# Kernel optimization log

Measured on AMD Instinct MI355X. Metric: run time of the kernel, lower is better.

The kernel has to match this reference:

```python
import jax, jax.numpy as jnp
import numpy as np

NEG_INF = -1e30  # stand-in for -inf pooling pad (matches torch max_pool2d implicit -inf pad)


def _max_pool(x, wh, ww, ph, pw):
    # x: (N, C, H, W); 'same'-style explicit padding as in torch max_pool2d
    return jax.lax.reduce_window(
        x, -jnp.inf, jax.lax.max,
        window_dimensions=(1, 1, wh, ww),
        window_strides=(1, 1, 1, 1),
        padding=((0, 0), (0, 0), (ph, ph), (pw, pw)))


def soft_erode(img):
    p1 = -_max_pool(-img, 3, 1, 1, 0)
    p2 = -_max_pool(-img, 1, 3, 0, 1)
    return jnp.minimum(p1, p2)


def soft_dilate(img):
    return _max_pool(img, 3, 3, 1, 1)


def soft_open(img):
    return soft_dilate(soft_erode(img))


def soft_skel(img, n_iter=50):
    skel = jax.nn.relu(img - soft_open(img))

    def body(carry, _):
        img, skel = carry
        img = soft_erode(img)
        delta = jax.nn.relu(img - soft_open(img))
        skel = skel + jax.nn.relu(delta - skel * delta)
        return (img, skel), None

    (_, skel), _ = jax.lax.scan(body, (img, skel), None, length=n_iter)
    return skel


def setup_inputs() -> dict:
    key = jax.random.key(0)
    k1, k2 = jax.random.split(key)
    N, C, H, W = 8, 1, 512, 512
    output = jax.random.normal(k1, (N, C, H, W), dtype=jnp.float32)
    target = jax.random.uniform(k2, (N, C, H, W), dtype=jnp.float32)
    return {"output": output, "target": target}


def reference(output, target):
    smooth = 1.0
    alpha = 0.7
    n_iter = 50
    axes = (1, 2, 3)  # per-sample reduction over C, H, W

    p = jax.nn.sigmoid(output)

    # soft clDice (vectorized over batch; original loops per sample with identical math)
    s_p = soft_skel(p, n_iter)
    s_l = soft_skel(target, n_iter)
    tprec = (jnp.sum(s_p * target, axes) + smooth) / (jnp.sum(s_p, axes) + smooth)
    tsens = (jnp.sum(s_l * p, axes) + smooth) / (jnp.sum(s_l, axes) + smooth)
    cl_dice = jnp.mean(1.0 - 2.0 * tprec * tsens / (tprec + tsens))

    # soft Dice
    inter = jnp.sum(p * target, axes)
    dice = jnp.mean(1.0 - 2.0 * (inter + smooth) /
                    (jnp.sum(p, axes) + jnp.sum(target, axes) + smooth))

    return alpha * dice + (1.0 - alpha) * cl_dice
```

## Files before the change

kernel.cpp:

```cpp
#include <hip/hip_runtime.h>
#include <math.h>

#define IMG   512
#define NSAMP 8
#define NIMG  16
#define PS    (IMG * IMG)

#define NBANDS 16
#define BH     (IMG / NBANDS)

__device__ __forceinline__ float sigm(float x) { return 1.0f / (1.0f + expf(-x)); }

__device__ __forceinline__ float dpp_a(float x) {
#if __has_builtin(__builtin_amdgcn_update_dpp)
    return __int_as_float(__builtin_amdgcn_update_dpp(0, __float_as_int(x),
                                                      0x130, 0xF, 0xF, true));
#else
    return __shfl_down(x, 1, 64);
#endif
}
__device__ __forceinline__ float dpp_b(float x) {
#if __has_builtin(__builtin_amdgcn_update_dpp)
    return __int_as_float(__builtin_amdgcn_update_dpp(0, __float_as_int(x),
                                                      0x138, 0xF, 0xF, true));
#else
    return __shfl_up(x, 1, 64);
#endif
}

__global__ __launch_bounds__(256) void prep_kernel(const float4* __restrict__ lg,
                                                   const float4* __restrict__ tg,
                                                   float4* __restrict__ X, int n4)
{
    int i = blockIdx.x * 256 + threadIdx.x;
    if (i < n4) {
        float4 L = lg[i];
        X[i]      = make_float4(sigm(L.x), sigm(L.y), sigm(L.z), sigm(L.w));
        X[i + n4] = tg[i];
    }
}

template<int C, bool ER, bool EC, bool INIT>
__device__ __forceinline__ void pipe_run(const float* __restrict__ xg,
                                         float* __restrict__ xo,
                                         float* __restrict__ Sg,
                                         int R0, int R1, int gcol, bool colOK, bool owned)
{
    const float INF = __builtin_inff();
    float A[C], B[C], HMA[C], HMB[C], SK[C];
    #pragma unroll
    for (int l = 0; l < C; ++l) {
        A[l] = INF; B[l] = INF; HMA[l] = -INF; HMB[l] = -INF; SK[l] = 0.f;
    }
    const int t0 = R0 - C - 1, t1 = R1 + C;

    auto xload = [&](int r) -> float {
        if (ER || EC) {
            bool ok = true;
            if (ER) ok = ok && ((unsigned)r < (unsigned)IMG);
            if (EC) ok = ok && colOK;
            float v = INF;
            if (ok) v = xg[r * IMG + gcol];
            return v;
        }
        return xg[r * IMG + gcol];
    };
    auto sload = [&](int r) -> float {
        if (INIT) return 0.f;
        if (ER || EC) {
            bool ok = true;
            if (ER) ok = ok && ((unsigned)r < (unsigned)IMG);
            if (EC) ok = ok && colOK;
            float v = 0.f;
            if (ok) v = Sg[r * IMG + gcol];
            return v;
        }
        return Sg[r * IMG + gcol];
    };

    float X0a = xload(t0), X0b = xload(t0 + 1);
    float SNa = sload(t0 - 1), SNb = sload(t0);

    #pragma unroll 2
    for (int t = t0; t <= t1; ++t) {
        float Cin = X0a; X0a = X0b; X0b = xload(t + 2);

        #pragma unroll
        for (int l = 0; l < C; ++l) {
            float Acur = A[l], Bcur = B[l];
            float e = fminf(fminf(Acur, Cin), Bcur);
            e = fminf(e, dpp_a(Bcur));
            e = fminf(e, dpp_b(Bcur));
            if (ER) e = ((unsigned)(t - l - 1) < (unsigned)IMG) ? e : INF;
            float eraw = e, xd = eraw;
            if (EC) {
                e  = colOK ? eraw :  INF;
                xd = colOK ? eraw : -INF;
            }
            float hm = fmaxf(xd, dpp_a(xd));
            hm = fmaxf(hm, dpp_b(xd));
            if (ER) hm = ((unsigned)(t - l - 1) < (unsigned)IMG) ? hm : -INF;
            float dil = fmaxf(fmaxf(HMA[l], HMB[l]), hm);
            float delta = fmaxf(Acur - dil, 0.f);
            float skl = SK[l];
            SK[l] = skl + fmaxf(delta - skl * delta, 0.f);
            A[l] = Bcur; B[l] = Cin;
            HMA[l] = HMB[l]; HMB[l] = hm;
            Cin = e;
        }

        int rx = t - C;
        if ((unsigned)(rx - R0) < (unsigned)(R1 - R0)) {
            if (owned) xo[rx * IMG + gcol] = Cin;
        }
        int rs = rx - 1;
        if ((unsigned)(rs - R0) < (unsigned)(R1 - R0)) {
            if (owned) Sg[rs * IMG + gcol] = SK[C - 1];
        }
        #pragma unroll
        for (int j = C - 1; j >= 1; --j) SK[j] = SK[j - 1];
        SK[0] = SNa; SNa = SNb; SNb = sload(t + 1);
    }
}

template<int C, bool INIT>
__global__ __launch_bounds__(256) void fused_pipe(const float* __restrict__ xin,
                                                  float* __restrict__ xout,
                                                  float* __restrict__ S)
{
    constexpr int OW = 64 - 2 * (C + 1);
    constexpr int NSTRIP = (IMG + OW - 1) / OW;
    const int lane = threadIdx.x & 63;
    const int task = blockIdx.x * 4 + (threadIdx.x >> 6);
    const int strip = task % NSTRIP;
    const int rem = task / NSTRIP;
    const int band = rem % NBANDS;
    const int img = rem / NBANDS;
    const int R0 = band * BH, R1 = R0 + BH;
    const int gcol = strip * OW - (C + 1) + lane;
    const bool colOK = (unsigned)gcol < (unsigned)IMG;
    const bool owned = (lane >= C + 1) && (lane < C + 1 + OW) && colOK;
    const float* xg = xin + (size_t)img * PS;
    float* xo = xout + (size_t)img * PS;
    float* Sg = S + (size_t)img * PS;
    const bool erow = (band == 0) || (band == NBANDS - 1);
    const bool ecol = (strip == 0) || (strip * OW - (C + 1) + 63 >= IMG);

    if (erow) {
        if (ecol) pipe_run<C, true , true , INIT>(xg, xo, Sg, R0, R1, gcol, colOK, owned);
        else      pipe_run<C, true , false, INIT>(xg, xo, Sg, R0, R1, gcol, colOK, owned);
    } else {
        if (ecol) pipe_run<C, false, true , INIT>(xg, xo, Sg, R0, R1, gcol, colOK, owned);
        else      pipe_run<C, false, false, INIT>(xg, xo, Sg, R0, R1, gcol, colOK, owned);
    }
}

__global__ __launch_bounds__(256) void reduce_kernel(const float* __restrict__ logits,
                                                     const float* __restrict__ target,
                                                     const float* __restrict__ S,
                                                     float* __restrict__ partial)
{
    const int sample = blockIdx.y;
    const size_t base = (size_t)sample * PS;
    const float4* p4  = (const float4*)(logits + base);
    const float4* t4  = (const float4*)(target + base);
    const float4* sp4 = (const float4*)(S + base);
    const float4* sl4 = (const float4*)(S + (size_t)NSAMP * PS + base);
    float v[7] = {0.f, 0.f, 0.f, 0.f, 0.f, 0.f, 0.f};
    const int n4 = PS / 4;
    for (int i = blockIdx.x * 256 + threadIdx.x; i < n4; i += 32 * 256) {
        float4 L = p4[i], Tt = t4[i], SP = sp4[i], SL = sl4[i];
        float p;
        p = sigm(L.x); v[0] += SP.x * Tt.x; v[1] += SP.x; v[2] += SL.x * p; v[3] += SL.x; v[4] += p * Tt.x; v[5] += p; v[6] += Tt.x;
        p = sigm(L.y); v[0] += SP.y * Tt.y; v[1] += SP.y; v[2] += SL.y * p; v[3] += SL.y; v[4] += p * Tt.y; v[5] += p; v[6] += Tt.y;
        p = sigm(L.z); v[0] += SP.z * Tt.z; v[1] += SP.z; v[2] += SL.z * p; v[3] += SL.z; v[4] += p * Tt.z; v[5] += p; v[6] += Tt.z;
        p = sigm(L.w); v[0] += SP.w * Tt.w; v[1] += SP.w; v[2] += SL.w * p; v[3] += SL.w; v[4] += p * Tt.w; v[5] += p; v[6] += Tt.w;
    }
    #pragma unroll
    for (int off = 32; off > 0; off >>= 1)
        #pragma unroll
        for (int q = 0; q < 7; ++q) v[q] += __shfl_down(v[q], off);
    __shared__ float wred[4][7];
    int lane = threadIdx.x & 63, w = threadIdx.x >> 6;
    if (lane == 0)
        #pragma unroll
        for (int q = 0; q < 7; ++q) wred[w][q] = v[q];
    __syncthreads();
    if (threadIdx.x == 0) {
        #pragma unroll
        for (int q = 0; q < 7; ++q)
            partial[(sample * 32 + blockIdx.x) * 7 + q] =
                wred[0][q] + wred[1][q] + wred[2][q] + wred[3][q];
    }
}

__global__ __launch_bounds__(256) void final_kernel(const float* __restrict__ partial,
                                                    float* __restrict__ out)
{
    const int t = threadIdx.x;
    const int sample = t >> 5, part = t & 31;
    float v[7];
    #pragma unroll
    for (int q = 0; q < 7; ++q) v[q] = partial[(sample * 32 + part) * 7 + q];
    #pragma unroll
    for (int off = 16; off > 0; off >>= 1)
        #pragma unroll
        for (int q = 0; q < 7; ++q) v[q] += __shfl_down(v[q], off, 32);
    __shared__ float acc[NSAMP][7];
    if (part == 0)
        #pragma unroll
        for (int q = 0; q < 7; ++q) acc[sample][q] = v[q];
    __syncthreads();
    if (t == 0) {
        float cl = 0.f, dice = 0.f;
        for (int n = 0; n < NSAMP; n++) {
            float A = acc[n][0], Bv = acc[n][1], Cc = acc[n][2], D = acc[n][3];
            float E = acc[n][4], F = acc[n][5], G = acc[n][6];
            float tprec = (A + 1.0f) / (Bv + 1.0f);
            float tsens = (Cc + 1.0f) / (D + 1.0f);
            cl   += 1.0f - 2.0f * tprec * tsens / (tprec + tsens);
            dice += 1.0f - 2.0f * (E + 1.0f) / (F + G + 1.0f);
        }
        out[0] = 0.7f * (dice / NSAMP) + 0.3f * (cl / NSAMP);
    }
}

extern "C" void kernel_launch(void* const* d_in, const int* in_sizes, int n_in,
                              void* d_out, int out_size, void* d_ws, size_t ws_size,
                              hipStream_t stream)
{
    const float* logits = (const float*)d_in[0];
    const float* target = (const float*)d_in[1];
    float* out = (float*)d_out;

    const size_t NTOT = (size_t)NIMG * PS;
    float* Xa = (float*)d_ws;
    float* Xb = Xa + NTOT;
    float* S  = Xb + NTOT;
    float* partial = S + NTOT;

    const int n4 = (NSAMP * PS) / 4;
    prep_kernel<<<n4 / 256, 256, 0, stream>>>((const float4*)logits, (const float4*)target,
                                              (float4*)Xa, n4);

    fused_pipe<6, true ><<<11 * 64, 256, 0, stream>>>(Xa, Xb, S);
    fused_pipe<5, false><<<10 * 64, 256, 0, stream>>>(Xb, Xa, S);
    fused_pipe<5, false><<<10 * 64, 256, 0, stream>>>(Xa, Xb, S);
    fused_pipe<5, false><<<10 * 64, 256, 0, stream>>>(Xb, Xa, S);
    fused_pipe<5, false><<<10 * 64, 256, 0, stream>>>(Xa, Xb, S);
    fused_pipe<5, false><<<10 * 64, 256, 0, stream>>>(Xb, Xa, S);
    fused_pipe<5, false><<<10 * 64, 256, 0, stream>>>(Xa, Xb, S);
    fused_pipe<5, false><<<10 * 64, 256, 0, stream>>>(Xb, Xa, S);
    fused_pipe<5, false><<<10 * 64, 256, 0, stream>>>(Xa, Xb, S);
    fused_pipe<5, false><<<10 * 64, 256, 0, stream>>>(Xb, Xa, S);

    reduce_kernel<<<dim3(32, NSAMP), 256, 0, stream>>>(logits, target, S, partial);
    final_kernel<<<1, 256, 0, stream>>>(partial, out);
}
```

Baseline: 343.1 us.

## Process two rows per step in fused erode/open pipeline with skeleton carry chain

```diff
diff --git a/kernel.cpp b/kernel.cpp
--- a/kernel.cpp
+++ b/kernel.cpp
@@ -44,33 +44,30 @@
 __device__ __forceinline__ void pipe_run(const float* __restrict__ xg,
                                          float* __restrict__ xo,
                                          float* __restrict__ Sg,
-                                         int R0, int R1, int gcol, bool colOK, bool owned)
+                                         int R0, int gcol, bool colOK, bool owned)
 {
     const float INF = __builtin_inff();
-    float A[C], B[C], HMA[C], HMB[C], SK[C];
+    float A[C], B[C], HMA[C], HMB[C], CARRY[C];
     #pragma unroll
     for (int l = 0; l < C; ++l) {
-        A[l] = INF; B[l] = INF; HMA[l] = -INF; HMB[l] = -INF; SK[l] = 0.f;
-    }
-    const int t0 = R0 - C - 1, t1 = R1 + C;
-
-    auto xload = [&](int r) -> float {
+        A[l] = INF; B[l] = INF; HMA[l] = -INF; HMB[l] = -INF; CARRY[l] = 0.f;
+    }
+    const int t0 = R0 - C - 1;
+    constexpr int NSTEPS = (BH + 2 * C + 2) / 2;
+
+    auto xld = [&](int r) -> float {
         if (ER || EC) {
-            bool ok = true;
-            if (ER) ok = ok && ((unsigned)r < (unsigned)IMG);
-            if (EC) ok = ok && colOK;
+            bool ok = (!ER || (unsigned)r < (unsigned)IMG) && (!EC || colOK);
             float v = INF;
             if (ok) v = xg[r * IMG + gcol];
             return v;
         }
         return xg[r * IMG + gcol];
     };
-    auto sload = [&](int r) -> float {
+    auto sld = [&](int r) -> float {
         if (INIT) return 0.f;
         if (ER || EC) {
-            bool ok = true;
-            if (ER) ok = ok && ((unsigned)r < (unsigned)IMG);
-            if (EC) ok = ok && colOK;
+            bool ok = (!ER || (unsigned)r < (unsigned)IMG) && (!EC || colOK);
             float v = 0.f;
             if (ok) v = Sg[r * IMG + gcol];
             return v;
@@ -78,48 +75,69 @@
         return Sg[r * IMG + gcol];
     };
 
-    float X0a = xload(t0), X0b = xload(t0 + 1);
-    float SNa = sload(t0 - 1), SNb = sload(t0);
+    float Xc0 = xld(t0),     Xc1 = xld(t0 + 1);
+    float Xn0 = xld(t0 + 2), Xn1 = xld(t0 + 3);
+    float Sc0 = sld(t0 - 2), Sc1 = sld(t0 - 1);
+    float Sn0 = sld(t0),     Sn1 = sld(t0 + 1);
 
     #pragma unroll 2
-    for (int t = t0; t <= t1; ++t) {
-        float Cin = X0a; X0a = X0b; X0b = xload(t + 2);
+    for (int k = 0; k < NSTEPS; ++k) {
+        const int t = t0 + 2 * k;
+        float Cin = Xc0, Din = Xc1;
+        float ska = Sc0, skb = Sc1;
+        Xc0 = Xn0; Xc1 = Xn1; Xn0 = xld(t + 4); Xn1 = xld(t + 5);
+        Sc0 = Sn0; Sc1 = Sn1; Sn0 = sld(t + 2); Sn1 = sld(t + 3);
+
+        float sk_a = 0.f, sk_b = 0.f;
 
         #pragma unroll
         for (int l = 0; l < C; ++l) {
             float Acur = A[l], Bcur = B[l];
-            float e = fminf(fminf(Acur, Cin), Bcur);
-            e = fminf(e, dpp_a(Bcur));
-            e = fminf(e, dpp_b(Bcur));
-            if (ER) e = ((unsigned)(t - l - 1) < (unsigned)IMG) ? e : INF;
-            float eraw = e, xd = eraw;
+            float v1 = fminf(fminf(Acur, Bcur), Cin);
+            float v2 = fminf(fminf(Bcur, Cin), Din);
+            float e1 = fminf(v1, fminf(dpp_a(Bcur), dpp_b(Bcur)));
+            float e2 = fminf(v2, fminf(dpp_a(Cin), dpp_b(Cin)));
+            if (ER) {
+                e1 = ((unsigned)(t - l - 1) < (unsigned)IMG) ? e1 : INF;
+                e2 = ((unsigned)(t - l)     < (unsigned)IMG) ? e2 : INF;
+            }
+            float xd1 = e1, xd2 = e2;
             if (EC) {
-                e  = colOK ? eraw :  INF;
-                xd = colOK ? eraw : -INF;
-            }
-            float hm = fmaxf(xd, dpp_a(xd));
-            hm = fmaxf(hm, dpp_b(xd));
-            if (ER) hm = ((unsigned)(t - l - 1) < (unsigned)IMG) ? hm : -INF;
-            float dil = fmaxf(fmaxf(HMA[l], HMB[l]), hm);
-            float delta = fmaxf(Acur - dil, 0.f);
-            float skl = SK[l];
-            SK[l] = skl + fmaxf(delta - skl * delta, 0.f);
-            A[l] = Bcur; B[l] = Cin;
-            HMA[l] = HMB[l]; HMB[l] = hm;
-            Cin = e;
-        }
-
-        int rx = t - C;
-        if ((unsigned)(rx - R0) < (unsigned)(R1 - R0)) {
-            if (owned) xo[rx * IMG + gcol] = Cin;
-        }
-        int rs = rx - 1;
-        if ((unsigned)(rs - R0) < (unsigned)(R1 - R0)) {
-            if (owned) Sg[rs * IMG + gcol] = SK[C - 1];
-        }
-        #pragma unroll
-        for (int j = C - 1; j >= 1; --j) SK[j] = SK[j - 1];
-        SK[0] = SNa; SNa = SNb; SNb = sload(t + 1);
+                xd1 = colOK ? e1 : -INF;  e1 = colOK ? e1 : INF;
+                xd2 = colOK ? e2 : -INF;  e2 = colOK ? e2 : INF;
+            }
+            float hm1 = fmaxf(xd1, fmaxf(dpp_a(xd1), dpp_b(xd1)));
+            float hm2 = fmaxf(xd2, fmaxf(dpp_a(xd2), dpp_b(xd2)));
+            if (ER) {
+                hm1 = ((unsigned)(t - l - 1) < (unsigned)IMG) ? hm1 : -INF;
+                hm2 = ((unsigned)(t - l)     < (unsigned)IMG) ? hm2 : -INF;
+            }
+            float dil1 = fmaxf(fmaxf(HMA[l], HMB[l]), hm1);
+            float dil2 = fmaxf(fmaxf(HMB[l], hm1), hm2);
+            float d1 = fmaxf(Acur - dil1, 0.f);
+            float d2 = fmaxf(Bcur - dil2, 0.f);
+            float so_a = ska + fmaxf(d1 - ska * d1, 0.f);
+            float so_b = skb + fmaxf(d2 - skb * d2, 0.f);
+            A[l] = Cin; B[l] = Din;
+            HMA[l] = hm1; HMB[l] = hm2;
+            Cin = e1; Din = e2;
+            if (l + 1 < C) {
+                float tmp = CARRY[l + 1];
+                CARRY[l + 1] = so_b;
+                ska = tmp;
+                skb = so_a;
+            } else {
+                sk_a = so_a; sk_b = so_b;
+            }
+        }
+
+        if (owned) {
+            int rs0 = t - C - 1, rs1 = t - C, rx1 = t - C + 1;
+            if ((unsigned)(rs0 - R0) < BH) Sg[rs0 * IMG + gcol] = sk_a;
+            if ((unsigned)(rs1 - R0) < BH) Sg[rs1 * IMG + gcol] = sk_b;
+            if ((unsigned)(rs1 - R0) < BH) xo[rs1 * IMG + gcol] = Cin;
+            if ((unsigned)(rx1 - R0) < BH) xo[rx1 * IMG + gcol] = Din;
+        }
     }
 }
 
@@ -136,7 +154,7 @@
     const int rem = task / NSTRIP;
     const int band = rem % NBANDS;
     const int img = rem / NBANDS;
-    const int R0 = band * BH, R1 = R0 + BH;
+    const int R0 = band * BH;
     const int gcol = strip * OW - (C + 1) + lane;
     const bool colOK = (unsigned)gcol < (unsigned)IMG;
     const bool owned = (lane >= C + 1) && (lane < C + 1 + OW) && colOK;
@@ -147,11 +165,11 @@
     const bool ecol = (strip == 0) || (strip * OW - (C + 1) + 63 >= IMG);
 
     if (erow) {
-        if (ecol) pipe_run<C, true , true , INIT>(xg, xo, Sg, R0, R1, gcol, colOK, owned);
-        else      pipe_run<C, true , false, INIT>(xg, xo, Sg, R0, R1, gcol, colOK, owned);
+        if (ecol) pipe_run<C, true , true , INIT>(xg, xo, Sg, R0, gcol, colOK, owned);
+        else      pipe_run<C, true , false, INIT>(xg, xo, Sg, R0, gcol, colOK, owned);
     } else {
-        if (ecol) pipe_run<C, false, true , INIT>(xg, xo, Sg, R0, R1, gcol, colOK, owned);
-        else      pipe_run<C, false, false, INIT>(xg, xo, Sg, R0, R1, gcol, colOK, owned);
+        if (ecol) pipe_run<C, false, true , INIT>(xg, xo, Sg, R0, gcol, colOK, owned);
+        else      pipe_run<C, false, false, INIT>(xg, xo, Sg, R0, gcol, colOK, owned);
     }
 }
 
```

Measured after the change: 369.4 us. +7.7%, slower.

## Double band count, rotate register queues, and skip final image store

Applied to the files above, without the earlier changes.

```diff
diff --git a/kernel.cpp b/kernel.cpp
--- a/kernel.cpp
+++ b/kernel.cpp
@@ -6,7 +6,7 @@
 #define NIMG  16
 #define PS    (IMG * IMG)
 
-#define NBANDS 16
+#define NBANDS 32
 #define BH     (IMG / NBANDS)
 
 __device__ __forceinline__ float sigm(float x) { return 1.0f / (1.0f + expf(-x)); }
@@ -40,93 +40,109 @@
     }
 }
 
-template<int C, bool ER, bool EC, bool INIT>
+template<int C, bool ER, bool EC, bool INIT, bool LAST>
 __device__ __forceinline__ void pipe_run(const float* __restrict__ xg,
                                          float* __restrict__ xo,
                                          float* __restrict__ Sg,
-                                         int R0, int R1, int gcol, bool colOK, bool owned)
+                                         int R0, int gcol, bool colOK, bool owned)
 {
     const float INF = __builtin_inff();
-    float A[C], B[C], HMA[C], HMB[C], SK[C];
+    constexpr int RAW    = BH + 2 * C + 2;
+    constexpr int INNER  = (C % 2 == 0) ? C : 2 * C;
+    constexpr int NSTEPS = ((RAW + INNER - 1) / INNER) * INNER;
+    constexpr int PAD    = NSTEPS - RAW;
+    constexpr int T0PAR  = (C + 1 + PAD) & 1;
+    constexpr int XS0    = 2 * C + 1 + PAD;
+    constexpr int SS0    = 2 * C + 2 + PAD;
+    const int t0 = R0 - C - 1 - PAD;
+
+    float W[C][2], HM[C][2], SK[C], XQ[C], SQ[C];
     #pragma unroll
     for (int l = 0; l < C; ++l) {
-        A[l] = INF; B[l] = INF; HMA[l] = -INF; HMB[l] = -INF; SK[l] = 0.f;
-    }
-    const int t0 = R0 - C - 1, t1 = R1 + C;
-
-    auto xload = [&](int r) -> float {
+        W[l][0] = INF;  W[l][1] = INF;
+        HM[l][0] = -INF; HM[l][1] = -INF;
+        SK[l] = 0.f;
+    }
+
+    const float* xp = xg + gcol;
+    float* sp = Sg + gcol;
+    float* op = xo + gcol;
+
+    auto xld = [&](int r) -> float {
         if (ER || EC) {
-            bool ok = true;
-            if (ER) ok = ok && ((unsigned)r < (unsigned)IMG);
-            if (EC) ok = ok && colOK;
+            bool ok = (!ER || (unsigned)r < (unsigned)IMG) && (!EC || colOK);
             float v = INF;
-            if (ok) v = xg[r * IMG + gcol];
+            if (ok) v = xp[r * IMG];
             return v;
         }
-        return xg[r * IMG + gcol];
+        return xp[r * IMG];
     };
-    auto sload = [&](int r) -> float {
+    auto sld = [&](int r) -> float {
         if (INIT) return 0.f;
         if (ER || EC) {
-            bool ok = true;
-            if (ER) ok = ok && ((unsigned)r < (unsigned)IMG);
-            if (EC) ok = ok && colOK;
+            bool ok = (!ER || (unsigned)r < (unsigned)IMG) && (!EC || colOK);
             float v = 0.f;
-            if (ok) v = Sg[r * IMG + gcol];
+            if (ok) v = sp[r * IMG];
             return v;
         }
-        return Sg[r * IMG + gcol];
+        return sp[r * IMG];
     };
 
-    float X0a = xload(t0), X0b = xload(t0 + 1);
-    float SNa = sload(t0 - 1), SNb = sload(t0);
-
-    #pragma unroll 2
-    for (int t = t0; t <= t1; ++t) {
-        float Cin = X0a; X0a = X0b; X0b = xload(t + 2);
-
-        #pragma unroll
-        for (int l = 0; l < C; ++l) {
-            float Acur = A[l], Bcur = B[l];
-            float e = fminf(fminf(Acur, Cin), Bcur);
-            e = fminf(e, dpp_a(Bcur));
-            e = fminf(e, dpp_b(Bcur));
-            if (ER) e = ((unsigned)(t - l - 1) < (unsigned)IMG) ? e : INF;
-            float eraw = e, xd = eraw;
-            if (EC) {
-                e  = colOK ? eraw :  INF;
-                xd = colOK ? eraw : -INF;
+    #pragma unroll
+    for (int i = 0; i < C; ++i) XQ[i] = xld(t0 + i);
+    #pragma unroll
+    for (int i = 0; i < C; ++i) SQ[i] = INIT ? 0.f : sld(t0 - 1 + i);
+
+    for (int kk = 0; kk < NSTEPS; kk += INNER) {
+        #pragma unroll
+        for (int j = 0; j < INNER; ++j) {
+            const int k = kk + j;
+            const int t = t0 + k;
+            const int qi = j % C;
+            float Cin = XQ[qi];
+            XQ[qi] = xld(t + C);
+            float snew = SQ[qi];
+            if (!INIT) SQ[qi] = sld(t + C - 1);
+
+            #pragma unroll
+            for (int l = 0; l < C; ++l) {
+                const int bp = (T0PAR + j + l + 1) & 1;
+                float Acur = W[l][bp ^ 1];
+                float Bcur = W[l][bp];
+                float e = fminf(fminf(Acur, Cin), Bcur);
+                e = fminf(e, dpp_a(Bcur));
+                e = fminf(e, dpp_b(Bcur));
+                if (ER) e = ((unsigned)(t - l - 1) < (unsigned)IMG) ? e : INF;
+                float xd = e;
+                if (EC) { xd = colOK ? e : -INF; e = colOK ? e : INF; }
+                float hm = fmaxf(xd, fmaxf(dpp_a(xd), dpp_b(xd)));
+                if (ER) hm = ((unsigned)(t - l - 1) < (unsigned)IMG) ? hm : -INF;
+                float dil = fmaxf(fmaxf(HM[l][bp], HM[l][bp ^ 1]), hm);
+                float d = fmaxf(Acur - dil, 0.f);
+                const int si = (l + C - qi) % C;
+                float skl = SK[si];
+                SK[si] = (skl + d) - skl * d;
+                W[l][bp ^ 1] = Cin;
+                HM[l][bp] = hm;
+                Cin = e;
             }
-            float hm = fmaxf(xd, dpp_a(xd));
-            hm = fmaxf(hm, dpp_b(xd));
-            if (ER) hm = ((unsigned)(t - l - 1) < (unsigned)IMG) ? hm : -INF;
-            float dil = fmaxf(fmaxf(HMA[l], HMB[l]), hm);
-            float delta = fmaxf(Acur - dil, 0.f);
-            float skl = SK[l];
-            SK[l] = skl + fmaxf(delta - skl * delta, 0.f);
-            A[l] = Bcur; B[l] = Cin;
-            HMA[l] = HMB[l]; HMB[l] = hm;
-            Cin = e;
-        }
-
-        int rx = t - C;
-        if ((unsigned)(rx - R0) < (unsigned)(R1 - R0)) {
-            if (owned) xo[rx * IMG + gcol] = Cin;
-        }
-        int rs = rx - 1;
-        if ((unsigned)(rs - R0) < (unsigned)(R1 - R0)) {
-            if (owned) Sg[rs * IMG + gcol] = SK[C - 1];
-        }
-        #pragma unroll
-        for (int j = C - 1; j >= 1; --j) SK[j] = SK[j - 1];
-        SK[0] = SNa; SNa = SNb; SNb = sload(t + 1);
-    }
-}
-
-template<int C, bool INIT>
-__global__ __launch_bounds__(256) void fused_pipe(const float* __restrict__ xin,
-                                                  float* __restrict__ xout,
-                                                  float* __restrict__ S)
+
+            if (!LAST) {
+                if ((unsigned)(k - XS0) < BH) { if (owned) op[(t - C) * IMG] = Cin; }
+            }
+            if ((unsigned)(k - SS0) < BH) {
+                const int so = (2 * C - 1 - qi) % C;
+                if (owned) sp[(t - C - 1) * IMG] = SK[so];
+            }
+            SK[(C - ((j + 1) % C)) % C] = snew;
+        }
+    }
+}
+
+template<int C, bool INIT, bool LAST>
+__global__ __launch_bounds__(256, 5) void fused_pipe(const float* __restrict__ xin,
+                                                     float* __restrict__ xout,
+                                                     float* __restrict__ S)
 {
     constexpr int OW = 64 - 2 * (C + 1);
     constexpr int NSTRIP = (IMG + OW - 1) / OW;
@@ -136,7 +152,7 @@
     const int rem = task / NSTRIP;
     const int band = rem % NBANDS;
     const int img = rem / NBANDS;
-    const int R0 = band * BH, R1 = R0 + BH;
+    const int R0 = band * BH;
     const int gcol = strip * OW - (C + 1) + lane;
     const bool colOK = (unsigned)gcol < (unsigned)IMG;
     const bool owned = (lane >= C + 1) && (lane < C + 1 + OW) && colOK;
@@ -147,11 +163,11 @@
     const bool ecol = (strip == 0) || (strip * OW - (C + 1) + 63 >= IMG);
 
     if (erow) {
-        if (ecol) pipe_run<C, true , true , INIT>(xg, xo, Sg, R0, R1, gcol, colOK, owned);
-        else      pipe_run<C, true , false, INIT>(xg, xo, Sg, R0, R1, gcol, colOK, owned);
+        if (ecol) pipe_run<C, true , true , INIT, LAST>(xg, xo, Sg, R0, gcol, colOK, owned);
+        else      pipe_run<C, true , false, INIT, LAST>(xg, xo, Sg, R0, gcol, colOK, owned);
     } else {
-        if (ecol) pipe_run<C, false, true , INIT>(xg, xo, Sg, R0, R1, gcol, colOK, owned);
-        else      pipe_run<C, false, false, INIT>(xg, xo, Sg, R0, R1, gcol, colOK, owned);
+        if (ecol) pipe_run<C, false, true , INIT, LAST>(xg, xo, Sg, R0, gcol, colOK, owned);
+        else      pipe_run<C, false, false, INIT, LAST>(xg, xo, Sg, R0, gcol, colOK, owned);
     }
 }
 
@@ -243,16 +259,18 @@
     prep_kernel<<<n4 / 256, 256, 0, stream>>>((const float4*)logits, (const float4*)target,
                                               (float4*)Xa, n4);
 
-    fused_pipe<6, true ><<<11 * 64, 256, 0, stream>>>(Xa, Xb, S);
-    fused_pipe<5, false><<<10 * 64, 256, 0, stream>>>(Xb, Xa, S);
-    fused_pipe<5, false><<<10 * 64, 256, 0, stream>>>(Xa, Xb, S);
-    fused_pipe<5, false><<<10 * 64, 256, 0, stream>>>(Xb, Xa, S);
-    fused_pipe<5, false><<<10 * 64, 256, 0, stream>>>(Xa, Xb, S);
-    fused_pipe<5, false><<<10 * 64, 256, 0, stream>>>(Xb, Xa, S);
-    fused_pipe<5, false><<<10 * 64, 256, 0, stream>>>(Xa, Xb, S);
-    fused_pipe<5, false><<<10 * 64, 256, 0, stream>>>(Xb, Xa, S);
-    fused_pipe<5, false><<<10 * 64, 256, 0, stream>>>(Xa, Xb, S);
-    fused_pipe<5, false><<<10 * 64, 256, 0, stream>>>(Xb, Xa, S);
+    const int B6 = 11 * NBANDS * NIMG / 4;
+    const int B5 = 10 * NBANDS * NIMG / 4;
+    fused_pipe<6, true , false><<<B6, 256, 0, stream>>>(Xa, Xb, S);
+    fused_pipe<5, false, false><<<B5, 256, 0, stream>>>(Xb, Xa, S);
+    fused_pipe<5, false, false><<<B5, 256, 0, stream>>>(Xa, Xb, S);
+    fused_pipe<5, false, false><<<B5, 256, 0, stream>>>(Xb, Xa, S);
+    fused_pipe<5, false, false><<<B5, 256, 0, stream>>>(Xa, Xb, S);
+    fused_pipe<5, false, false><<<B5, 256, 0, stream>>>(Xb, Xa, S);
+    fused_pipe<5, false, false><<<B5, 256, 0, stream>>>(Xa, Xb, S);
+    fused_pipe<5, false, false><<<B5, 256, 0, stream>>>(Xb, Xa, S);
+    fused_pipe<5, false, false><<<B5, 256, 0, stream>>>(Xa, Xb, S);
+    fused_pipe<5, false, true ><<<B5, 256, 0, stream>>>(Xb, Xa, S);
 
     reduce_kernel<<<dim3(32, NSAMP), 256, 0, stream>>>(logits, target, S, partial);
     final_kernel<<<1, 256, 0, stream>>>(partial, out);
```

Result: slower. 624.8 us (+82.1%).
